# Performance work log

Measured on AMD Instinct MI355X. Metric: run time of the kernel, lower is better.

Reference implementation:

```python
import jax, jax.numpy as jnp
import numpy as np

B, S, DIM = 1, 2048, 4096
N_HEADS, N_KV_HEADS = 32, 8
HEAD_DIM = DIM // N_HEADS            # 128
N_REP = N_HEADS // N_KV_HEADS        # 4
Q_SIZE = N_HEADS * HEAD_DIM          # 4096
KV_SIZE = N_KV_HEADS * HEAD_DIM      # 1024


def setup_inputs() -> dict:
    key = jax.random.key(0)
    ks = jax.random.split(key, 5)
    x = jax.random.normal(ks[0], (B, S, DIM), dtype=jnp.float32)
    # RoPE tables: freqs_cis[s, j] = exp(i * s * theta_j), theta_j = 10000^(-2j/head_dim)
    theta = 10000.0 ** (-jnp.arange(0, HEAD_DIM, 2, dtype=jnp.float32) / HEAD_DIM)
    ang = jnp.arange(S, dtype=jnp.float32)[:, None] * theta[None, :]  # [S, HEAD_DIM//2]
    freqs_cos = jnp.cos(ang)
    freqs_sin = jnp.sin(ang)
    # causal additive mask [1,1,S,S]
    causal = jnp.tril(jnp.ones((S, S), dtype=bool))
    mask = jnp.where(causal, 0.0, -1e9).astype(jnp.float32)[None, None]
    wqkv = jax.random.normal(ks[1], (Q_SIZE + 2 * KV_SIZE, DIM), dtype=jnp.float32) * (DIM ** -0.5)
    wo = jax.random.normal(ks[2], (DIM, Q_SIZE), dtype=jnp.float32) * (Q_SIZE ** -0.5)
    return {"x": x, "freqs_cos": freqs_cos, "freqs_sin": freqs_sin, "mask": mask,
            "wqkv": wqkv, "wo": wo}


def _apply_rope(t, cos, sin):
    # t: [B, S, H, D]; cos/sin: [S, D//2]  (complex multiply on (even, odd) pairs)
    b, s, h, d = t.shape
    tp = t.reshape(b, s, h, d // 2, 2)
    t0, t1 = tp[..., 0], tp[..., 1]
    c = cos[None, :, None, :]
    sn = sin[None, :, None, :]
    out = jnp.stack([t0 * c - t1 * sn, t0 * sn + t1 * c], axis=-1)
    return out.reshape(b, s, h, d)


def reference(x, freqs_cos, freqs_sin, mask, wqkv, wo):
    bsz, seqlen, _ = x.shape
    qkv = jnp.einsum('bsd,od->bso', x, wqkv)  # fused QKV projection
    xq = qkv[..., :Q_SIZE].reshape(bsz, seqlen, N_HEADS, HEAD_DIM)
    xk = qkv[..., Q_SIZE:Q_SIZE + KV_SIZE].reshape(bsz, seqlen, N_KV_HEADS, HEAD_DIM)
    xv = qkv[..., Q_SIZE + KV_SIZE:].reshape(bsz, seqlen, N_KV_HEADS, HEAD_DIM)
    # rotary embedding on q, k
    xq = _apply_rope(xq, freqs_cos, freqs_sin)
    xk = _apply_rope(xk, freqs_cos, freqs_sin)
    # cache insertion (prefill: cache == current k/v), layout [B, KVH, S, D]
    cache_k = jnp.swapaxes(xk, 1, 2)
    cache_v = jnp.swapaxes(xv, 1, 2)
    # GQA repeat_kv -> [B, H, S, D]
    keys = jnp.repeat(cache_k, N_REP, axis=1)
    values = jnp.repeat(cache_v, N_REP, axis=1)
    # scores: einsum 'ijkl,ikml->ikjm' with xq [b,s,h,d], keys [b,h,t,d] -> [b,h,s,t]
    scores = jnp.einsum('bshd,bhtd->bhst', xq, keys) / jnp.sqrt(jnp.float32(HEAD_DIM))
    scores = scores + mask
    scores = jax.nn.softmax(scores.astype(jnp.float32), axis=-1).astype(xq.dtype)
    out = jnp.einsum('bhst,bhtd->bhsd', scores, values)  # [B, H, S, D]
    out = jnp.swapaxes(out, 1, 2).reshape(bsz, seqlen, Q_SIZE)
    return jnp.einsum('bso,do->bsd', out, wo)
```

## Files before the change

kernel.cpp:

```cpp
#include <hip/hip_runtime.h>
#include <hip/hip_bf16.h>
#include <cstdint>
#include <cstddef>


typedef __attribute__((ext_vector_type(4)))  float    f32x4;
typedef __attribute__((ext_vector_type(16))) float    f32x16;
typedef __attribute__((ext_vector_type(8)))  __bf16   bf16x8;
typedef __attribute__((ext_vector_type(4)))  __bf16   bf16x4;
typedef __attribute__((ext_vector_type(2)))  __bf16   bf16x2;
typedef __attribute__((ext_vector_type(4)))  uint32_t u32x4;

typedef const __attribute__((address_space(1))) void* gaddr_t;
typedef __attribute__((address_space(3))) void*       laddr_t;

#define S_LEN   2048
#define DIM_    4096
#define NHEADS  32
#define NKV     8
#define HD      128
#define QKV_LD  6144
#define KOFF    4096
#define VOFF    5120

#define EXP2F(x) __builtin_amdgcn_exp2f(x)

#define N4_X  2097152
#define N4_W  6291456
#define N4_O  4194304
__global__ void cvt3(const float* __restrict__ x, __bf16* __restrict__ xb,
                     const float* __restrict__ wq, __bf16* __restrict__ wqb,
                     const float* __restrict__ wo, __bf16* __restrict__ wob) {
  int idx = blockIdx.x * blockDim.x + threadIdx.x;
  int stride = gridDim.x * blockDim.x;
  for (int i = idx; i < N4_X + N4_W + N4_O; i += stride) {
    const float* src; __bf16* dst; int k;
    if (i < N4_X)            { src = x;  dst = xb;  k = i; }
    else if (i < N4_X + N4_W){ src = wq; dst = wqb; k = i - N4_X; }
    else                     { src = wo; dst = wob; k = i - N4_X - N4_W; }
    float4 v = reinterpret_cast<const float4*>(src)[k];
    bf16x4 o;
    o[0] = (__bf16)v.x; o[1] = (__bf16)v.y; o[2] = (__bf16)v.z; o[3] = (__bf16)v.w;
    reinterpret_cast<bf16x4*>(dst)[k] = o;
  }
}

__global__ void rope_kernel(__bf16* __restrict__ qkv, const float* __restrict__ fc,
                            const float* __restrict__ fs) {
  int tid = blockIdx.x * 256 + threadIdx.x;
  int i = tid & 63;
  int t = tid >> 6;
  int h = t % 40;
  int s = t / 40;
  int col = (h < NHEADS) ? (h * HD + 2 * i) : (KOFF + (h - NHEADS) * HD + 2 * i);
  size_t off = (size_t)s * QKV_LD + col;
  float c = fc[s * 64 + i], sn = fs[s * 64 + i];
  bf16x2 v = *reinterpret_cast<bf16x2*>(&qkv[off]);
  float t0 = (float)v[0], t1 = (float)v[1];
  bf16x2 o;
  o[0] = (__bf16)(t0 * c - t1 * sn);
  o[1] = (__bf16)(t0 * sn + t1 * c);
  *reinterpret_cast<bf16x2*>(&qkv[off]) = o;
}

__device__ __forceinline__ void stg64(const __bf16* __restrict__ P, int ld, int row0,
                                      int kt, char* dst, int tid) {
  int r = tid >> 3, g = tid & 7;
  int row = row0 + r;
  const __bf16* src = P + (size_t)row * ld + kt * 64 + ((g ^ (row & 7)) * 8);
  __builtin_amdgcn_global_load_lds((gaddr_t)src,
      (laddr_t)(dst + (tid & ~63) * 16), 16, 0, 0);
}

template <int QM, int QN, bool RA, bool RB, int VW>
__device__ __forceinline__ void g1_phase(const __bf16* __restrict__ Ab,
                                         const __bf16* __restrict__ Bb,
                                         f32x4 (&acc)[8][4],
                                         bf16x8 (&afr)[4][2], bf16x8 (&bfr)[2][2],
                                         int wm, int wn, int l15, int hi, int tid,
                                         const __bf16* __restrict__ SP, int sld,
                                         int srow, int skt, char* sdst, bool doSt) {
  if constexpr (RA) {
#pragma unroll
    for (int fm = 0; fm < 4; ++fm) {
      int R = wm * 128 + QM * 64 + fm * 16 + l15;
#pragma unroll
      for (int kk = 0; kk < 2; ++kk)
        afr[fm][kk] = *reinterpret_cast<const bf16x8*>(
            (const char*)Ab + R * 128 + (((kk * 4 + hi) ^ (R & 7)) * 16));
    }
  }
  if constexpr (RB) {
#pragma unroll
    for (int fn = 0; fn < 2; ++fn) {
      int R = wn * 64 + QN * 32 + fn * 16 + l15;
#pragma unroll
      for (int kk = 0; kk < 2; ++kk)
        bfr[fn][kk] = *reinterpret_cast<const bf16x8*>(
            (const char*)Bb + R * 128 + (((kk * 4 + hi) ^ (R & 7)) * 16));
    }
  }
  if (doSt) {
    stg64(SP, sld, srow, skt, sdst, tid);
    stg64(SP, sld, srow + 64, skt, sdst + 8192, tid);
  }
  __builtin_amdgcn_s_barrier();
  asm volatile("s_waitcnt lgkmcnt(0)" ::: "memory");
  __builtin_amdgcn_sched_barrier(0);
  __builtin_amdgcn_s_setprio(1);
#pragma unroll
  for (int kk = 0; kk < 2; ++kk)
#pragma unroll
    for (int fm = 0; fm < 4; ++fm)
#pragma unroll
      for (int fn = 0; fn < 2; ++fn)
        acc[QM * 4 + fm][QN * 2 + fn] = __builtin_amdgcn_mfma_f32_16x16x32_bf16(
            afr[fm][kk], bfr[fn][kk], acc[QM * 4 + fm][QN * 2 + fn], 0, 0, 0);
  __builtin_amdgcn_s_setprio(0);
  if constexpr (VW == 4) asm volatile("s_waitcnt vmcnt(4)" ::: "memory");
  if constexpr (VW == 0) asm volatile("s_waitcnt vmcnt(0)" ::: "memory");
  __builtin_amdgcn_s_barrier();
}

__global__ __launch_bounds__(512) void g1_8p(const __bf16* __restrict__ A,
                                             const __bf16* __restrict__ B,
                                             __bf16* __restrict__ C, int K,
                                             int lda, int ldb, int ldc) {
  __shared__ __align__(16) __bf16 As[2][256 * 64];
  __shared__ __align__(16) __bf16 Bs[2][256 * 64];
  const int tid = threadIdx.x;
  const int l15 = tid & 15, hi = (tid >> 4) & 3, w = tid >> 6;
  const int wm = w >> 2, wn = w & 3;
  const int bid = blockIdx.x, xcd = bid & 7, lid = bid >> 3;
  const int m0 = (lid % 8) * 256;
  const int n0 = (xcd * 3 + lid / 8) * 256;

  f32x4 acc[8][4] = {};
  bf16x8 afr[4][2], bfr[2][2];
  char* A0 = (char*)As[0]; char* A1 = (char*)As[1];
  char* B0 = (char*)Bs[0]; char* B1 = (char*)Bs[1];

  stg64(A, lda, m0,       0, A0,         tid); stg64(A, lda, m0 + 64,  0, A0 + 8192,  tid);
  stg64(B, ldb, n0,       0, B0,         tid); stg64(B, ldb, n0 + 64,  0, B0 + 8192,  tid);
  stg64(A, lda, m0 + 128, 0, A0 + 16384, tid); stg64(A, lda, m0 + 192, 0, A0 + 24576, tid);
  stg64(B, ldb, n0 + 128, 0, B0 + 16384, tid); stg64(B, ldb, n0 + 192, 0, B0 + 24576, tid);
  stg64(A, lda, m0,       1, A1,         tid); stg64(A, lda, m0 + 64,  1, A1 + 8192,  tid);
  stg64(B, ldb, n0 + 128, 1, B1 + 16384, tid); stg64(B, ldb, n0 + 192, 1, B1 + 24576, tid);
  asm volatile("s_waitcnt vmcnt(4)" ::: "memory");
  __builtin_amdgcn_s_barrier();

  const int nt = K >> 6;
  for (int it = 0; it < nt; it += 2) {
    const bool sB = (it + 2 < nt), sC = (it + 3 < nt);
    const bool last = !sB;
    const __bf16* Ab0 = As[0]; const __bf16* Bb0 = Bs[0];
    const __bf16* Ab1 = As[1]; const __bf16* Bb1 = Bs[1];
    g1_phase<0, 0, true,  true, -1>(Ab0, Bb0, acc, afr, bfr, wm, wn, l15, hi, tid,
                                    A, lda, m0 + 128, it + 1, A1 + 16384, true);
    g1_phase<0, 1, false, true, -1>(Ab0, Bb0, acc, afr, bfr, wm, wn, l15, hi, tid,
                                    B, ldb, n0, it + 1, B1, true);
    g1_phase<1, 1, true, false, -1>(Ab0, Bb0, acc, afr, bfr, wm, wn, l15, hi, tid,
                                    A, lda, m0, it + 2, A0, sB);
    if (last)
      g1_phase<1, 0, false, true, 0>(Ab0, Bb0, acc, afr, bfr, wm, wn, l15, hi, tid,
                                     B, ldb, n0 + 128, it + 2, B0 + 16384, sB);
    else
      g1_phase<1, 0, false, true, 4>(Ab0, Bb0, acc, afr, bfr, wm, wn, l15, hi, tid,
                                     B, ldb, n0 + 128, it + 2, B0 + 16384, sB);
    g1_phase<0, 0, true,  true, -1>(Ab1, Bb1, acc, afr, bfr, wm, wn, l15, hi, tid,
                                    A, lda, m0 + 128, it + 2, A0 + 16384, sB);
    g1_phase<0, 1, false, true, -1>(Ab1, Bb1, acc, afr, bfr, wm, wn, l15, hi, tid,
                                    B, ldb, n0, it + 2, B0, sB);
    g1_phase<1, 1, true, false, -1>(Ab1, Bb1, acc, afr, bfr, wm, wn, l15, hi, tid,
                                    A, lda, m0, it + 3, A1, sC);
    if (last)
      g1_phase<1, 0, false, true, 0>(Ab1, Bb1, acc, afr, bfr, wm, wn, l15, hi, tid,
                                     B, ldb, n0 + 128, it + 3, B1 + 16384, sC);
    else
      g1_phase<1, 0, false, true, 4>(Ab1, Bb1, acc, afr, bfr, wm, wn, l15, hi, tid,
                                     B, ldb, n0 + 128, it + 3, B1 + 16384, sC);
  }

#pragma unroll
  for (int qm = 0; qm < 2; ++qm)
#pragma unroll
    for (int fm = 0; fm < 4; ++fm)
#pragma unroll
      for (int qn = 0; qn < 2; ++qn)
#pragma unroll
        for (int fn = 0; fn < 2; ++fn)
#pragma unroll
          for (int j = 0; j < 4; ++j) {
            int row = m0 + wm * 128 + qm * 64 + fm * 16 + hi * 4 + j;
            int col = n0 + wn * 64 + qn * 32 + fn * 16 + l15;
            C[(size_t)row * ldc + col] = (__bf16)acc[qm * 4 + fm][qn * 2 + fn][j];
          }
}

template <int MW, int NW, int KH, int NST, bool VM>
__device__ __forceinline__ void phase32(const __bf16* __restrict__ Ab,
                                        const __bf16* __restrict__ Bb,
                                        f32x16 (&acc)[MW][NW],
                                        int wm, int wn, int l31, int hi, int tid,
                                        const __bf16* __restrict__ SP, int sld,
                                        int srow0, char* sdst, int kt, bool st) {
  bf16x8 af[MW][2], bfr[NW][2];
#pragma unroll
  for (int mi = 0; mi < MW; ++mi) {
    int R = wm * (MW * 32) + mi * 32 + l31;
#pragma unroll
    for (int k2 = 0; k2 < 2; ++k2)
      af[mi][k2] = *reinterpret_cast<const bf16x8*>(
          (const char*)Ab + R * 128 + (((KH * 4 + k2 * 2 + hi) ^ (R & 7)) * 16));
  }
#pragma unroll
  for (int ni = 0; ni < NW; ++ni) {
    int R = wn * (NW * 32) + ni * 32 + l31;
#pragma unroll
    for (int k2 = 0; k2 < 2; ++k2)
      bfr[ni][k2] = *reinterpret_cast<const bf16x8*>(
          (const char*)Bb + R * 128 + (((KH * 4 + k2 * 2 + hi) ^ (R & 7)) * 16));
  }
  if (st) {
#pragma unroll
    for (int h = 0; h < NST; ++h)
      stg64(SP, sld, srow0 + h * 64, kt, sdst + h * 8192, tid);
  }
  __builtin_amdgcn_s_barrier();
  asm volatile("s_waitcnt lgkmcnt(0)" ::: "memory");
  __builtin_amdgcn_sched_barrier(0);
  __builtin_amdgcn_s_setprio(1);
#pragma unroll
  for (int k2 = 0; k2 < 2; ++k2)
#pragma unroll
    for (int mi = 0; mi < MW; ++mi)
#pragma unroll
      for (int ni = 0; ni < NW; ++ni)
        acc[mi][ni] = __builtin_amdgcn_mfma_f32_32x32x16_bf16(af[mi][k2], bfr[ni][k2],
                                                              acc[mi][ni], 0, 0, 0);
  __builtin_amdgcn_s_setprio(0);
  if (VM) asm volatile("s_waitcnt vmcnt(0)" ::: "memory");
  __builtin_amdgcn_s_barrier();
}

template <int BM, int BN, int MB, int NPX, typename OutT>
__global__ __launch_bounds__(512) void gemm32(const __bf16* __restrict__ A,
                                              const __bf16* __restrict__ B,
                                              OutT* __restrict__ C, int K,
                                              int lda, int ldb, int ldc) {
  constexpr int MW = BM / 64;
  constexpr int NW = BN / 128;
  constexpr int AST = BM / 64, BST = BN / 64;
  __shared__ __align__(16) __bf16 As[2][BM * 64];
  __shared__ __align__(16) __bf16 Bs[2][BN * 64];
  const int tid = threadIdx.x;
  const int lane = tid & 63, l31 = lane & 31, hi = lane >> 5, w = tid >> 6;
  const int wm = w >> 2, wn = w & 3;
  const int bid = blockIdx.x, xcd = bid & 7, lid = bid >> 3;
  const int m0 = (lid % MB) * BM;
  const int n0 = (xcd * NPX + lid / MB) * BN;

  f32x16 acc[MW][NW] = {};

#pragma unroll
  for (int h = 0; h < AST; ++h) stg64(A, lda, m0 + h * 64, 0, (char*)As[0] + h * 8192, tid);
#pragma unroll
  for (int h = 0; h < BST; ++h) stg64(B, ldb, n0 + h * 64, 0, (char*)Bs[0] + h * 8192, tid);
  asm volatile("s_waitcnt vmcnt(0)" ::: "memory");
  __builtin_amdgcn_s_barrier();

  const int ntiles = K >> 6;
  for (int t = 0; t < ntiles; ++t) {
    const int cur = t & 1;
    const __bf16* Ab = As[cur];
    const __bf16* Bb = Bs[cur];
    char* dA = (char*)As[1 - cur];
    char* dB = (char*)Bs[1 - cur];
    const bool st = (t + 1 < ntiles);
    phase32<MW, NW, 0, AST, false>(Ab, Bb, acc, wm, wn, l31, hi, tid,
                                   A, lda, m0, dA, t + 1, st);
    phase32<MW, NW, 1, BST, true >(Ab, Bb, acc, wm, wn, l31, hi, tid,
                                   B, ldb, n0, dB, t + 1, st);
  }

#pragma unroll
  for (int mi = 0; mi < MW; ++mi)
#pragma unroll
    for (int ni = 0; ni < NW; ++ni)
#pragma unroll
      for (int e = 0; e < 16; ++e) {
        int row = m0 + wm * (MW * 32) + mi * 32 + (e & 3) + 8 * (e >> 2) + 4 * hi;
        int col = n0 + wn * (NW * 32) + ni * 32 + l31;
        C[(size_t)row * ldc + col] = (OutT)acc[mi][ni][e];
      }
}

__device__ inline uint32_t pack2(float a, float b) {
  bf16x2 t; t[0] = (__bf16)a; t[1] = (__bf16)b;
  return __builtin_bit_cast(uint32_t, t);
}

__global__ __launch_bounds__(256, 2) void attn_kernel(const __bf16* __restrict__ qkv,
                                                      __bf16* __restrict__ out) {
  __shared__ __align__(16) __bf16 Ks[2][64 * 128];
  __shared__ __align__(16) __bf16 Vt[2][128][66];
  const int tid = threadIdx.x;
  const int lane = tid & 63, l31 = lane & 31, hi = lane >> 5, wq = tid >> 6;
  const int head = blockIdx.x & 31;
  const int g = blockIdx.x >> 5;
  const int qt = (g < 8) ? (15 - g) : (g - 8);
  const int q0 = qt * 128;
  const int nt = 2 * qt + 2;
  const int kvh = head >> 2;
  const float sc2 = 0.08838834764831845f * 1.44269504089f;
  const int qr = q0 + wq * 32 + l31;

  bf16x8 vr[2][2];

  auto stage_k = [&](int tt, int buf) {
#pragma unroll
    for (int i = 0; i < 4; ++i) {
      int c = i * 256 + tid;
      int r = c >> 4, gg = c & 15;
      const __bf16* gk = qkv + (size_t)(tt * 64 + r) * QKV_LD + KOFF + kvh * HD + ((gg ^ (r & 7)) * 8);
      __builtin_amdgcn_global_load_lds((gaddr_t)gk,
          (laddr_t)((char*)Ks[buf] + (tid & ~63) * 16 + i * 4096), 16, 0, 0);
    }
  };
  auto load_v = [&](int tt) {
#pragma unroll
    for (int i = 0; i < 2; ++i) {
      int task = i * 256 + tid;
      int p = task >> 4, cg = task & 15;
      const __bf16* vp = qkv + (size_t)(tt * 64 + 2 * p) * QKV_LD + VOFF + kvh * HD + cg * 8;
      vr[i][0] = *reinterpret_cast<const bf16x8*>(vp);
      vr[i][1] = *reinterpret_cast<const bf16x8*>(vp + QKV_LD);
    }
  };
  auto write_v = [&](int buf) {
#pragma unroll
    for (int i = 0; i < 2; ++i) {
      int task = i * 256 + tid;
      int p = task >> 4, cg = task & 15;
#pragma unroll
      for (int e = 0; e < 8; ++e) {
        bf16x2 pkv; pkv[0] = vr[i][0][e]; pkv[1] = vr[i][1][e];
        *reinterpret_cast<bf16x2*>(&Vt[buf][cg * 8 + e][2 * p]) = pkv;
      }
    }
  };

  bf16x8 qf[8];
  {
    const __bf16* qp = qkv + (size_t)qr * QKV_LD + head * HD + hi * 8;
#pragma unroll
    for (int ks = 0; ks < 8; ++ks) qf[ks] = *reinterpret_cast<const bf16x8*>(qp + ks * 16);
  }
  f32x16 o[4] = {};
  float m_run = -3e38f, l_run = 0.f;

  stage_k(0, 0); load_v(0); write_v(0);

  for (int t = 0; t < nt; ++t) {
    const int cur = t & 1;
    __syncthreads();
    if (t + 1 < nt) { stage_k(t + 1, 1 - cur); load_v(t + 1); }

    f32x16 st[2];
    __builtin_amdgcn_s_setprio(1);
#pragma unroll
    for (int sub = 0; sub < 2; ++sub) {
      f32x16 acc = {};
      int r = sub * 32 + l31;
#pragma unroll
      for (int ks = 0; ks < 8; ++ks) {
        int gg = (ks * 2 + hi) ^ (r & 7);
        bf16x8 kf = *reinterpret_cast<const bf16x8*>((char*)Ks[cur] + r * 256 + gg * 16);
        acc = __builtin_amdgcn_mfma_f32_32x32x16_bf16(kf, qf[ks], acc, 0, 0, 0);
      }
      st[sub] = acc;
    }
    __builtin_amdgcn_s_setprio(0);
    if (t >= nt - 2) {
      const int kv0 = t * 64;
#pragma unroll
      for (int sub = 0; sub < 2; ++sub)
#pragma unroll
        for (int e = 0; e < 16; ++e) {
          int kvg = kv0 + sub * 32 + (e & 3) + 8 * (e >> 2) + 4 * hi;
          if (kvg > qr) st[sub][e] = -1e30f;
        }
    }
    float pm = st[0][0];
#pragma unroll
    for (int e = 1; e < 16; ++e) pm = fmaxf(pm, st[0][e]);
#pragma unroll
    for (int e = 0; e < 16; ++e) pm = fmaxf(pm, st[1][e]);
    pm = fmaxf(pm, __shfl_xor(pm, 32));
    pm *= sc2;
    if (!__all(pm - m_run <= 8.f)) {
      float mn = fmaxf(m_run, pm);
      float fsc = EXP2F(m_run - mn);
      m_run = mn;
      l_run *= fsc;
#pragma unroll
      for (int dt = 0; dt < 4; ++dt)
#pragma unroll
        for (int e = 0; e < 16; ++e) o[dt][e] *= fsc;
    }
    float rs = 0.f;
#pragma unroll
    for (int sub = 0; sub < 2; ++sub)
#pragma unroll
      for (int e = 0; e < 16; ++e) {
        float p = EXP2F(__builtin_fmaf(st[sub][e], sc2, -m_run));
        st[sub][e] = p;
        rs += p;
      }
    rs += __shfl_xor(rs, 32);
    l_run += rs;

    uint32_t pk[16];
#pragma unroll
    for (int sub = 0; sub < 2; ++sub)
#pragma unroll
      for (int i = 0; i < 8; ++i)
        pk[sub * 8 + i] = pack2(st[sub][2 * i], st[sub][2 * i + 1]);
    uint32_t rv[8];
#pragma unroll
    for (int m = 0; m < 8; ++m) {
      int base = 4 * (m >> 1) + (m & 1);
      uint32_t snd = hi ? pk[base] : pk[base + 2];
      rv[m] = __shfl_xor(snd, 32);
    }
    bf16x8 pf[4];
#pragma unroll
    for (int tt = 0; tt < 4; ++tt) {
      u32x4 wv;
      wv[0] = hi ? rv[2 * tt]     : pk[4 * tt];
      wv[1] = hi ? rv[2 * tt + 1] : pk[4 * tt + 1];
      wv[2] = hi ? pk[4 * tt + 2] : rv[2 * tt];
      wv[3] = hi ? pk[4 * tt + 3] : rv[2 * tt + 1];
      pf[tt] = __builtin_bit_cast(bf16x8, wv);
    }
    __builtin_amdgcn_s_setprio(1);
#pragma unroll
    for (int dt = 0; dt < 4; ++dt) {
      int dr = dt * 32 + l31;
#pragma unroll
      for (int tt = 0; tt < 4; ++tt) {
        bf16x8 vf = *reinterpret_cast<const bf16x8*>((char*)&Vt[cur][0][0] + dr * 132 + tt * 32 + hi * 16);
        o[dt] = __builtin_amdgcn_mfma_f32_32x32x16_bf16(vf, pf[tt], o[dt], 0, 0, 0);
      }
    }
    __builtin_amdgcn_s_setprio(0);
    if (t + 1 < nt) write_v(1 - cur);
  }

  float inv = 1.f / l_run;
  __bf16* scr = &Ks[0][0] + wq * 1280;
  const int qq = lane >> 1, part = lane & 1;
#pragma unroll
  for (int dt = 0; dt < 4; ++dt) {
    __syncthreads();
#pragma unroll
    for (int i = 0; i < 8; ++i) {
      int d0 = (2 * i & 3) + 8 * (i >> 1) + 4 * hi;
      bf16x2 prr;
      prr[0] = (__bf16)(o[dt][2 * i] * inv);
      prr[1] = (__bf16)(o[dt][2 * i + 1] * inv);
      *reinterpret_cast<bf16x2*>(scr + l31 * 40 + d0) = prr;
    }
    __syncthreads();
    bf16x8 r0 = *reinterpret_cast<const bf16x8*>(scr + qq * 40 + part * 16);
    bf16x8 r1 = *reinterpret_cast<const bf16x8*>(scr + qq * 40 + part * 16 + 8);
    __bf16* op = out + (size_t)(q0 + wq * 32 + qq) * DIM_ + head * HD + dt * 32 + part * 16;
    *reinterpret_cast<bf16x8*>(op) = r0;
    *reinterpret_cast<bf16x8*>(op + 8) = r1;
  }
}

extern "C" void kernel_launch(void* const* d_in, const int* in_sizes, int n_in,
                              void* d_out, int out_size, void* d_ws, size_t ws_size,
                              hipStream_t stream) {
  (void)in_sizes; (void)n_in; (void)out_size; (void)ws_size;
  const float* x    = (const float*)d_in[0];
  const float* fc   = (const float*)d_in[1];
  const float* fs   = (const float*)d_in[2];
  const float* wqkv = (const float*)d_in[4];
  const float* wo   = (const float*)d_in[5];
  float* out = (float*)d_out;

  char* ws = (char*)d_ws;
  __bf16* xb    = (__bf16*)(ws);
  __bf16* wqkvb = (__bf16*)(ws + 16777216);
  __bf16* wob   = (__bf16*)(ws + 67108864);
  __bf16* qkv   = (__bf16*)(ws + 100663296);
  __bf16* attnO = xb;

  cvt3<<<2048, 256, 0, stream>>>(x, xb, wqkv, wqkvb, wo, wob);

  g1_8p<<<192, 512, 0, stream>>>(xb, wqkvb, qkv, DIM_, DIM_, DIM_, QKV_LD);

  rope_kernel<<<(S_LEN * 40 * 64) / 256, 256, 0, stream>>>(qkv, fc, fs);

  attn_kernel<<<512, 256, 0, stream>>>(qkv, attnO);

  gemm32<128, 256, 16, 2, float><<<256, 512, 0, stream>>>(attnO, wob, out, DIM_, DIM_, DIM_, DIM_);
}
```

Baseline: 326.3 us.

## Replace output-projection GEMM with 8-phase pipelined 16x16x32 MFMA kernel

Replaces the generic gemm32 output-projection kernel with a specialized g2_8p kernel. It uses 16x16x32 bf16 MFMAs over quarter-tiles and reuses A/B fragments across phases. Global-to-LDS staging is split into finer chunks spread across eight phases per two K-tiles, with partial vmcnt waits so loads overlap compute more deeply. This is meant to hide memory latency and reduce LDS fragment reloads, at the cost of more barriers and more complex staging logic.

```diff
diff --git a/kernel.cpp b/kernel.cpp
--- a/kernel.cpp
+++ b/kernel.cpp
@@ -197,102 +197,130 @@
           }
 }
 
-template <int MW, int NW, int KH, int NST, bool VM>
-__device__ __forceinline__ void phase32(const __bf16* __restrict__ Ab,
-                                        const __bf16* __restrict__ Bb,
-                                        f32x16 (&acc)[MW][NW],
-                                        int wm, int wn, int l31, int hi, int tid,
-                                        const __bf16* __restrict__ SP, int sld,
-                                        int srow0, char* sdst, int kt, bool st) {
-  bf16x8 af[MW][2], bfr[NW][2];
-#pragma unroll
-  for (int mi = 0; mi < MW; ++mi) {
-    int R = wm * (MW * 32) + mi * 32 + l31;
-#pragma unroll
-    for (int k2 = 0; k2 < 2; ++k2)
-      af[mi][k2] = *reinterpret_cast<const bf16x8*>(
-          (const char*)Ab + R * 128 + (((KH * 4 + k2 * 2 + hi) ^ (R & 7)) * 16));
-  }
-#pragma unroll
-  for (int ni = 0; ni < NW; ++ni) {
-    int R = wn * (NW * 32) + ni * 32 + l31;
-#pragma unroll
-    for (int k2 = 0; k2 < 2; ++k2)
-      bfr[ni][k2] = *reinterpret_cast<const bf16x8*>(
-          (const char*)Bb + R * 128 + (((KH * 4 + k2 * 2 + hi) ^ (R & 7)) * 16));
-  }
-  if (st) {
-#pragma unroll
-    for (int h = 0; h < NST; ++h)
-      stg64(SP, sld, srow0 + h * 64, kt, sdst + h * 8192, tid);
+template <int QM, int QN, bool RA, bool RB, int VW, int NS>
+__device__ __forceinline__ void g2_phase(const __bf16* __restrict__ Ab,
+                                         const __bf16* __restrict__ Bb,
+                                         f32x4 (&acc)[4][4],
+                                         bf16x8 (&afr)[2][2], bf16x8 (&bfr)[2][2],
+                                         int wm, int wn, int l15, int hi, int tid,
+                                         const __bf16* __restrict__ SP, int sld,
+                                         int srow, int skt, char* sdst, bool doSt) {
+  if constexpr (RA) {
+#pragma unroll
+    for (int fm = 0; fm < 2; ++fm) {
+      int R = wm * 64 + QM * 32 + fm * 16 + l15;
+#pragma unroll
+      for (int kk = 0; kk < 2; ++kk)
+        afr[fm][kk] = *reinterpret_cast<const bf16x8*>(
+            (const char*)Ab + R * 128 + (((kk * 4 + hi) ^ (R & 7)) * 16));
+    }
+  }
+  if constexpr (RB) {
+#pragma unroll
+    for (int fn = 0; fn < 2; ++fn) {
+      int R = wn * 64 + QN * 32 + fn * 16 + l15;
+#pragma unroll
+      for (int kk = 0; kk < 2; ++kk)
+        bfr[fn][kk] = *reinterpret_cast<const bf16x8*>(
+            (const char*)Bb + R * 128 + (((kk * 4 + hi) ^ (R & 7)) * 16));
+    }
+  }
+  if (doSt) {
+#pragma unroll
+    for (int s = 0; s < NS; ++s)
+      stg64(SP, sld, srow + s * 64, skt, sdst + s * 8192, tid);
   }
   __builtin_amdgcn_s_barrier();
   asm volatile("s_waitcnt lgkmcnt(0)" ::: "memory");
   __builtin_amdgcn_sched_barrier(0);
   __builtin_amdgcn_s_setprio(1);
 #pragma unroll
-  for (int k2 = 0; k2 < 2; ++k2)
-#pragma unroll
-    for (int mi = 0; mi < MW; ++mi)
-#pragma unroll
-      for (int ni = 0; ni < NW; ++ni)
-        acc[mi][ni] = __builtin_amdgcn_mfma_f32_32x32x16_bf16(af[mi][k2], bfr[ni][k2],
-                                                              acc[mi][ni], 0, 0, 0);
+  for (int kk = 0; kk < 2; ++kk)
+#pragma unroll
+    for (int fm = 0; fm < 2; ++fm)
+#pragma unroll
+      for (int fn = 0; fn < 2; ++fn)
+        acc[QM * 2 + fm][QN * 2 + fn] = __builtin_amdgcn_mfma_f32_16x16x32_bf16(
+            afr[fm][kk], bfr[fn][kk], acc[QM * 2 + fm][QN * 2 + fn], 0, 0, 0);
   __builtin_amdgcn_s_setprio(0);
-  if (VM) asm volatile("s_waitcnt vmcnt(0)" ::: "memory");
+  if constexpr (VW == 3) asm volatile("s_waitcnt vmcnt(3)" ::: "memory");
+  if constexpr (VW == 0) asm volatile("s_waitcnt vmcnt(0)" ::: "memory");
   __builtin_amdgcn_s_barrier();
 }
 
-template <int BM, int BN, int MB, int NPX, typename OutT>
-__global__ __launch_bounds__(512) void gemm32(const __bf16* __restrict__ A,
-                                              const __bf16* __restrict__ B,
-                                              OutT* __restrict__ C, int K,
-                                              int lda, int ldb, int ldc) {
-  constexpr int MW = BM / 64;
-  constexpr int NW = BN / 128;
-  constexpr int AST = BM / 64, BST = BN / 64;
-  __shared__ __align__(16) __bf16 As[2][BM * 64];
-  __shared__ __align__(16) __bf16 Bs[2][BN * 64];
+__global__ __launch_bounds__(512) void g2_8p(const __bf16* __restrict__ A,
+                                             const __bf16* __restrict__ B,
+                                             float* __restrict__ C, int K,
+                                             int lda, int ldb, int ldc) {
+  __shared__ __align__(16) __bf16 As[2][128 * 64];
+  __shared__ __align__(16) __bf16 Bs[2][256 * 64];
   const int tid = threadIdx.x;
-  const int lane = tid & 63, l31 = lane & 31, hi = lane >> 5, w = tid >> 6;
+  const int l15 = tid & 15, hi = (tid >> 4) & 3, w = tid >> 6;
   const int wm = w >> 2, wn = w & 3;
   const int bid = blockIdx.x, xcd = bid & 7, lid = bid >> 3;
-  const int m0 = (lid % MB) * BM;
-  const int n0 = (xcd * NPX + lid / MB) * BN;
-
-  f32x16 acc[MW][NW] = {};
-
-#pragma unroll
-  for (int h = 0; h < AST; ++h) stg64(A, lda, m0 + h * 64, 0, (char*)As[0] + h * 8192, tid);
-#pragma unroll
-  for (int h = 0; h < BST; ++h) stg64(B, ldb, n0 + h * 64, 0, (char*)Bs[0] + h * 8192, tid);
-  asm volatile("s_waitcnt vmcnt(0)" ::: "memory");
+  const int m0 = (lid % 16) * 128;
+  const int n0 = (xcd * 2 + lid / 16) * 256;
+
+  f32x4 acc[4][4] = {};
+  bf16x8 afr[2][2], bfr[2][2];
+  char* A0 = (char*)As[0]; char* A1 = (char*)As[1];
+  char* B0 = (char*)Bs[0]; char* B1 = (char*)Bs[1];
+
+  stg64(A, lda, m0,       0, A0,         tid);
+  stg64(B, ldb, n0,       0, B0,         tid); stg64(B, ldb, n0 + 64,  0, B0 + 8192,  tid);
+  stg64(A, lda, m0 + 64,  0, A0 + 8192,  tid);
+  stg64(B, ldb, n0 + 128, 0, B0 + 16384, tid); stg64(B, ldb, n0 + 192, 0, B0 + 24576, tid);
+  stg64(A, lda, m0,       1, A1,         tid);
+  stg64(B, ldb, n0 + 128, 1, B1 + 16384, tid); stg64(B, ldb, n0 + 192, 1, B1 + 24576, tid);
+  asm volatile("s_waitcnt vmcnt(3)" ::: "memory");
   __builtin_amdgcn_s_barrier();
 
-  const int ntiles = K >> 6;
-  for (int t = 0; t < ntiles; ++t) {
-    const int cur = t & 1;
-    const __bf16* Ab = As[cur];
-    const __bf16* Bb = Bs[cur];
-    char* dA = (char*)As[1 - cur];
-    char* dB = (char*)Bs[1 - cur];
-    const bool st = (t + 1 < ntiles);
-    phase32<MW, NW, 0, AST, false>(Ab, Bb, acc, wm, wn, l31, hi, tid,
-                                   A, lda, m0, dA, t + 1, st);
-    phase32<MW, NW, 1, BST, true >(Ab, Bb, acc, wm, wn, l31, hi, tid,
-                                   B, ldb, n0, dB, t + 1, st);
-  }
-
-#pragma unroll
-  for (int mi = 0; mi < MW; ++mi)
-#pragma unroll
-    for (int ni = 0; ni < NW; ++ni)
-#pragma unroll
-      for (int e = 0; e < 16; ++e) {
-        int row = m0 + wm * (MW * 32) + mi * 32 + (e & 3) + 8 * (e >> 2) + 4 * hi;
-        int col = n0 + wn * (NW * 32) + ni * 32 + l31;
-        C[(size_t)row * ldc + col] = (OutT)acc[mi][ni][e];
-      }
+  const int nt = K >> 6;
+  for (int it = 0; it < nt; it += 2) {
+    const bool sB = (it + 2 < nt), sC = (it + 3 < nt);
+    const bool last = !sB;
+    const __bf16* Ab0 = As[0]; const __bf16* Bb0 = Bs[0];
+    const __bf16* Ab1 = As[1]; const __bf16* Bb1 = Bs[1];
+    g2_phase<0, 0, true,  true, -1, 1>(Ab0, Bb0, acc, afr, bfr, wm, wn, l15, hi, tid,
+                                       A, lda, m0 + 64, it + 1, A1 + 8192, true);
+    g2_phase<0, 1, false, true, -1, 2>(Ab0, Bb0, acc, afr, bfr, wm, wn, l15, hi, tid,
+                                       B, ldb, n0, it + 1, B1, true);
+    g2_phase<1, 1, true, false, -1, 1>(Ab0, Bb0, acc, afr, bfr, wm, wn, l15, hi, tid,
+                                       A, lda, m0, it + 2, A0, sB);
+    if (last)
+      g2_phase<1, 0, false, true, 0, 2>(Ab0, Bb0, acc, afr, bfr, wm, wn, l15, hi, tid,
+                                        B, ldb, n0 + 128, it + 2, B0 + 16384, sB);
+    else
+      g2_phase<1, 0, false, true, 3, 2>(Ab0, Bb0, acc, afr, bfr, wm, wn, l15, hi, tid,
+                                        B, ldb, n0 + 128, it + 2, B0 + 16384, sB);
+    g2_phase<0, 0, true,  true, -1, 1>(Ab1, Bb1, acc, afr, bfr, wm, wn, l15, hi, tid,
+                                       A, lda, m0 + 64, it + 2, A0 + 8192, sB);
+    g2_phase<0, 1, false, true, -1, 2>(Ab1, Bb1, acc, afr, bfr, wm, wn, l15, hi, tid,
+                                       B, ldb, n0, it + 2, B0, sB);
+    g2_phase<1, 1, true, false, -1, 1>(Ab1, Bb1, acc, afr, bfr, wm, wn, l15, hi, tid,
+                                       A, lda, m0, it + 3, A1, sC);
+    if (last)
+      g2_phase<1, 0, false, true, 0, 2>(Ab1, Bb1, acc, afr, bfr, wm, wn, l15, hi, tid,
+                                        B, ldb, n0 + 128, it + 3, B1 + 16384, sC);
+    else
+      g2_phase<1, 0, false, true, 3, 2>(Ab1, Bb1, acc, afr, bfr, wm, wn, l15, hi, tid,
+                                        B, ldb, n0 + 128, it + 3, B1 + 16384, sC);
+  }
+
+#pragma unroll
+  for (int qm = 0; qm < 2; ++qm)
+#pragma unroll
+    for (int fm = 0; fm < 2; ++fm)
+#pragma unroll
+      for (int qn = 0; qn < 2; ++qn)
+#pragma unroll
+        for (int fn = 0; fn < 2; ++fn)
+#pragma unroll
+          for (int j = 0; j < 4; ++j) {
+            int row = m0 + wm * 64 + qm * 32 + fm * 16 + hi * 4 + j;
+            int col = n0 + wn * 64 + qn * 32 + fn * 16 + l15;
+            C[(size_t)row * ldc + col] = acc[qm * 2 + fm][qn * 2 + fn][j];
+          }
 }
 
 __device__ inline uint32_t pack2(float a, float b) {
@@ -506,5 +534,5 @@
 
   attn_kernel<<<512, 256, 0, stream>>>(qkv, attnO);
 
-  gemm32<128, 256, 16, 2, float><<<256, 512, 0, stream>>>(attnO, wob, out, DIM_, DIM_, DIM_, DIM_);
-}
+  g2_8p<<<256, 512, 0, stream>>>(attnO, wob, out, DIM_, DIM_, DIM_, DIM_);
+}
```

New measurement: 321.4 us. About the same (-1.5%).
